# Optimization experiments

Hardware: AMD Instinct MI355X
Metric: run time of the kernel (lower is better)

## Reference

```python
import jax, jax.numpy as jnp
import numpy as np
from jax import lax

N = 100000      # nodes
F_IN = 128      # dataset.num_features
H = 64          # hidden
E = 1600000     # edges
G = 1000        # graphs (equal-sized, contiguous)
PER = N // G    # nodes per graph = 100
K = 30          # sort-pool k
KS = 3          # conv1d kernel = num_layers


def setup_inputs() -> dict:
    key = jax.random.key(0)
    ks = jax.random.split(key, 20)
    lin = lambda k, i, o: (jax.random.normal(k, (i, o), jnp.float32) / np.sqrt(i)).astype(jnp.float32)
    return {
        "x": jax.random.normal(ks[0], (N, F_IN), jnp.float32),
        "src": jax.random.randint(ks[1], (E,), 0, N, dtype=jnp.int32),
        "dst": jax.random.randint(ks[2], (E,), 0, N, dtype=jnp.int32),
        "num_graphs": G,
        # SAGEConv 1: lin_l (aggr, with bias), lin_r (self, no bias)
        "wl1": lin(ks[3], F_IN, H), "wr1": lin(ks[4], F_IN, H), "b1": jnp.zeros((H,), jnp.float32),
        "wl2": lin(ks[5], H, H), "wr2": lin(ks[6], H, H), "b2": jnp.zeros((H,), jnp.float32),
        "wl3": lin(ks[7], H, H), "wr3": lin(ks[8], H, H), "b3": jnp.zeros((H,), jnp.float32),
        # Conv1d(hidden=64 -> 32, kernel=3): weight [O, I, K]
        "cw": (jax.random.normal(ks[9], (32, H, KS), jnp.float32) / np.sqrt(H * KS)).astype(jnp.float32),
        "cb": jnp.zeros((32,), jnp.float32),
        "w1": lin(ks[10], 32 * (K - KS + 1), H), "bb1": jnp.zeros((H,), jnp.float32),
        "w2": lin(ks[11], H, 1), "bb2": jnp.zeros((1,), jnp.float32),
    }


def _sage(x, src, dst, wl, wr, b, n):
    # PyG SAGEConv (mean aggr): lin_l(mean_{j->i} x_j) + lin_r(x_i)
    msum = jax.ops.segment_sum(x[src], dst, num_segments=n)           # [N, F]
    cnt = jax.ops.segment_sum(jnp.ones((src.shape[0],), x.dtype), dst, num_segments=n)
    mean = msum / jnp.maximum(cnt, 1.0)[:, None]
    return mean @ wl + b + x @ wr


def reference(x, src, dst, num_graphs, wl1, wr1, b1, wl2, wr2, b2, wl3, wr3, b3, cw, cb, w1, bb1, w2, bb2):
    n = x.shape[0]
    h = jax.nn.relu(_sage(x, src, dst, wl1, wr1, b1, n))
    h = jax.nn.relu(_sage(h, src, dst, wl2, wr2, b2, n))
    h = jax.nn.relu(_sage(h, src, dst, wl3, wr3, b3, n))
    # SortAggregation(k): per-graph, sort nodes by last feature channel (desc), keep top-k.
    # batch = contiguous equal-sized graphs -> dense reshape is exact.
    hg = h.reshape(num_graphs, PER, H)                                # [G, PER, H]
    order = jnp.argsort(-hg[:, :, -1], axis=1)[:, :K]                 # [G, K]
    topk = jnp.take_along_axis(hg, order[:, :, None], axis=1)         # [G, K, H]
    xc = jnp.transpose(topk, (0, 2, 1))                               # [G, H, K]
    y = lax.conv_general_dilated(xc, cw, (1,), 'VALID',
                                 dimension_numbers=('NCH', 'OIH', 'NCH'))
    y = jax.nn.relu(y + cb[None, :, None])                            # [G, 32, K-KS+1]
    y = y.reshape(num_graphs, -1)
    y = jax.nn.relu(y @ w1 + bb1)
    # dropout: eval mode -> identity
    return y @ w2 + bb2                                               # [G, 1]
```

## Files before the change

kernel.cpp:

```cpp
#include <hip/hip_runtime.h>

#define NN 100000
#define EE 1600000
#define GG 1000
#define PERG 100
#define KK 30
#define HH 64

#define NB 782
#define CAP 4096
#define CHB 4096
#define BUCKET_BLOCKS ((EE + CHB - 1) / CHB)
#define PROJ_BLOCKS ((NN + 127) / 128)
#define LAYER_BLOCKS ((NN + 63) / 64)

__device__ __forceinline__ void bucket_body(int bid, float* smem,
                                            const int* __restrict__ src,
                                            const int* __restrict__ dst,
                                            int* __restrict__ gcur,
                                            int* __restrict__ pairs) {
  int* lhist = (int*)smem;
  int* lbase = lhist + NB;
  int* lcur = lbase + NB;
  const int t = threadIdx.x;
  const int c0 = bid * CHB;
  const int c1 = min(c0 + CHB, EE);
  for (int b = t; b < NB; b += 256) {
    lhist[b] = 0;
    lcur[b] = 0;
  }
  __syncthreads();
  for (int e = c0 + t; e < c1; e += 256) atomicAdd(&lhist[dst[e] >> 7], 1);
  __syncthreads();
  for (int b = t; b < NB; b += 256) {
    int c = lhist[b];
    lbase[b] = c ? atomicAdd(&gcur[b], c) : 0;
  }
  __syncthreads();
  for (int e = c0 + t; e < c1; e += 256) {
    int d = dst[e];
    int b = d >> 7;
    int p = atomicAdd(&lcur[b], 1);
    pairs[b * CAP + lbase[b] + p] = (src[e] << 7) | (d & 127);
  }
}

template <int K>
__device__ __forceinline__ void proj_body(int bid, float* smem,
                                          const float* __restrict__ X,
                                          const float* __restrict__ WL,
                                          const float* __restrict__ WR,
                                          float* __restrict__ P,
                                          float* __restrict__ R) {
  constexpr int BM = 128, BK = 32, XSP = 36, WSP = 144;
  float* xs = smem;
  float* ws = smem + BM * XSP;
  const int t = threadIdx.x;
  const int row0 = bid * BM;
  const int tc = t & 15, tr = t >> 4;
  const int wcol = tc * 8 + (tc >> 2) * 4;

  float acc[8][8];
#pragma unroll
  for (int i = 0; i < 8; ++i)
#pragma unroll
    for (int j = 0; j < 8; ++j) acc[i][j] = 0.f;

  for (int k0 = 0; k0 < K; k0 += BK) {
    __syncthreads();
    for (int idx = t; idx < BM * 8; idx += 256) {
      int r = idx >> 3, c = idx & 7;
      int row = row0 + r;
      float4 v = make_float4(0.f, 0.f, 0.f, 0.f);
      if (row < NN) v = *reinterpret_cast<const float4*>(&X[(size_t)row * K + k0 + c * 4]);
      *reinterpret_cast<float4*>(&xs[r * XSP + c * 4]) = v;
    }
    for (int idx = t; idx < BK * 16; idx += 256) {
      int kr = idx >> 4, c4 = idx & 15;
      int gcl = c4 >> 1;
      int off = gcl * 8 + (gcl >> 2) * 4 + (c4 & 1) * 4;
      *reinterpret_cast<float4*>(&ws[kr * WSP + off]) =
          *reinterpret_cast<const float4*>(&WL[(k0 + kr) * 64 + c4 * 4]);
      int g2 = gcl + 8;
      int off2 = g2 * 8 + (g2 >> 2) * 4 + (c4 & 1) * 4;
      *reinterpret_cast<float4*>(&ws[kr * WSP + off2]) =
          *reinterpret_cast<const float4*>(&WR[(k0 + kr) * 64 + c4 * 4]);
    }
    __syncthreads();
    for (int kk4 = 0; kk4 < BK; kk4 += 4) {
      float4 a[8];
#pragma unroll
      for (int i = 0; i < 8; ++i)
        a[i] = *reinterpret_cast<const float4*>(&xs[(tr + 16 * i) * XSP + kk4]);
#pragma unroll
      for (int kk = 0; kk < 4; ++kk) {
        float4 b0 = *reinterpret_cast<const float4*>(&ws[(kk4 + kk) * WSP + wcol]);
        float4 b1 = *reinterpret_cast<const float4*>(&ws[(kk4 + kk) * WSP + wcol + 4]);
        float bv[8] = {b0.x, b0.y, b0.z, b0.w, b1.x, b1.y, b1.z, b1.w};
#pragma unroll
        for (int i = 0; i < 8; ++i) {
          float av = (kk == 0) ? a[i].x : (kk == 1) ? a[i].y : (kk == 2) ? a[i].z : a[i].w;
#pragma unroll
          for (int j = 0; j < 8; ++j) acc[i][j] = fmaf(av, bv[j], acc[i][j]);
        }
      }
    }
  }

  float* OUT = (tc < 8) ? P : R;
  int cb = (tc & 7) * 8;
#pragma unroll
  for (int i = 0; i < 8; ++i) {
    int row = row0 + tr + 16 * i;
    if (row < NN) {
      *reinterpret_cast<float4*>(&OUT[(size_t)row * 64 + cb]) =
          make_float4(acc[i][0], acc[i][1], acc[i][2], acc[i][3]);
      *reinterpret_cast<float4*>(&OUT[(size_t)row * 64 + cb + 4]) =
          make_float4(acc[i][4], acc[i][5], acc[i][6], acc[i][7]);
    }
  }
}

__global__ __launch_bounds__(256) void fused_bucket_proj(const int* __restrict__ src,
                                                         const int* __restrict__ dst,
                                                         int* __restrict__ gcur,
                                                         int* __restrict__ pairs,
                                                         const float* __restrict__ X,
                                                         const float* __restrict__ WL,
                                                         const float* __restrict__ WR,
                                                         float* __restrict__ P,
                                                         float* __restrict__ R) {
  __shared__ float smem[128 * 36 + 32 * 144];
  if (blockIdx.x < PROJ_BLOCKS)
    proj_body<128>(blockIdx.x, smem, X, WL, WR, P, R);
  else
    bucket_body(blockIdx.x - PROJ_BLOCKS, smem, src, dst, gcur, pairs);
}

__global__ __launch_bounds__(256) void csr_kernel(const int* __restrict__ gcur,
                                                  const int* __restrict__ pairs,
                                                  int* __restrict__ row_start,
                                                  int* __restrict__ cnt,
                                                  int* __restrict__ eidx) {
  __shared__ int vals[CAP];
  __shared__ int hist[128];
  __shared__ int offs[128];
  __shared__ int cur[128];
  __shared__ int red[4];
  const int b = blockIdx.x;
  const int t = threadIdx.x;
  int s = 0;
  for (int i = t; i < b; i += 256) s += gcur[i];
#pragma unroll
  for (int off = 32; off > 0; off >>= 1) s += __shfl_xor(s, off);
  if ((t & 63) == 0) red[t >> 6] = s;
  if (t < 128) {
    hist[t] = 0;
    cur[t] = 0;
  }
  __syncthreads();
  const int base = red[0] + red[1] + red[2] + red[3];
  const int nb = gcur[b];
  for (int i = t; i < nb; i += 256) {
    int v = pairs[b * CAP + i];
    vals[i] = v;
    atomicAdd(&hist[v & 127], 1);
  }
  __syncthreads();
  if (t < 128) {
    int ss = 0;
    for (int m = 0; m < t; ++m) ss += hist[m];
    offs[t] = ss;
    int node = b * 128 + t;
    if (node < NN) {
      row_start[node] = base + ss;
      cnt[node] = hist[t];
    }
  }
  __syncthreads();
  for (int i = t; i < nb; i += 256) {
    int v = vals[i];
    int ld = v & 127;
    int p = atomicAdd(&cur[ld], 1);
    eidx[base + offs[ld] + p] = v >> 7;
  }
}

__global__ __launch_bounds__(256) void layer_kernel(const float* __restrict__ P,
                                                    const float* __restrict__ R,
                                                    const float* __restrict__ bias,
                                                    const int* __restrict__ row_start,
                                                    const int* __restrict__ cnt,
                                                    const int* __restrict__ eidx,
                                                    const float* __restrict__ WL,
                                                    const float* __restrict__ WR,
                                                    float* __restrict__ Pout,
                                                    float* __restrict__ Rout,
                                                    float* __restrict__ keyP,
                                                    float* __restrict__ keyR) {
  __shared__ float hs[64 * 68];
  const int t = threadIdx.x;
  const int lane = t & 63;
  const int qd = t >> 4;
  const int ql = t & 15;
  const int row0 = blockIdx.x * 64;

  for (int p = 0; p < 4; ++p) {
    const int r = qd + 16 * p;
    const int node = row0 + r;
    float4 acc = make_float4(0.f, 0.f, 0.f, 0.f);
    if (node < NN) {
      const int base = row_start[node];
      const int deg = cnt[node];
      for (int e0 = 0; e0 < deg; e0 += 16) {
        const int rem = deg - e0;
        const int ii = (ql < rem) ? ql : (rem - 1);
        int idx = eidx[base + e0 + ii];
#pragma unroll
        for (int j = 0; j < 16; ++j) {
          const int sj = __shfl(idx, (lane & 48) | j);
          const float wj = (j < rem) ? 1.f : 0.f;
          const float4 vj = *reinterpret_cast<const float4*>(&P[(size_t)sj * 64 + ql * 4]);
          acc.x = fmaf(wj, vj.x, acc.x);
          acc.y = fmaf(wj, vj.y, acc.y);
          acc.z = fmaf(wj, vj.z, acc.z);
          acc.w = fmaf(wj, vj.w, acc.w);
        }
      }
      const float dv = fmaxf((float)deg, 1.0f);
      const float4 r4 = *reinterpret_cast<const float4*>(&R[(size_t)node * 64 + ql * 4]);
      const float4 b4 = *reinterpret_cast<const float4*>(&bias[ql * 4]);
      acc.x = fmaxf(acc.x / dv + b4.x + r4.x, 0.f);
      acc.y = fmaxf(acc.y / dv + b4.y + r4.y, 0.f);
      acc.z = fmaxf(acc.z / dv + b4.z + r4.z, 0.f);
      acc.w = fmaxf(acc.w / dv + b4.w + r4.w, 0.f);
    }
    *reinterpret_cast<float4*>(&hs[r * 68 + ql * 4]) = acc;
  }
  __syncthreads();

  const int tc = t & 15, tr = t >> 4;
  const float* WB = (tc < 8) ? WL : WR;
  const int wcolg = (tc & 7) * 8;

  float acc[4][8];
#pragma unroll
  for (int i = 0; i < 4; ++i)
#pragma unroll
    for (int j = 0; j < 8; ++j) acc[i][j] = 0.f;

  for (int kk4 = 0; kk4 < 64; kk4 += 4) {
    float4 a[4];
#pragma unroll
    for (int i = 0; i < 4; ++i)
      a[i] = *reinterpret_cast<const float4*>(&hs[(tr + 16 * i) * 68 + kk4]);
#pragma unroll
    for (int kk = 0; kk < 4; ++kk) {
      float4 b0 = *reinterpret_cast<const float4*>(&WB[(kk4 + kk) * 64 + wcolg]);
      float4 b1 = *reinterpret_cast<const float4*>(&WB[(kk4 + kk) * 64 + wcolg + 4]);
      float bv[8] = {b0.x, b0.y, b0.z, b0.w, b1.x, b1.y, b1.z, b1.w};
#pragma unroll
      for (int i = 0; i < 4; ++i) {
        float av = (kk == 0) ? a[i].x : (kk == 1) ? a[i].y : (kk == 2) ? a[i].z : a[i].w;
#pragma unroll
        for (int j = 0; j < 8; ++j) acc[i][j] = fmaf(av, bv[j], acc[i][j]);
      }
    }
  }

  float* OUT = (tc < 8) ? Pout : Rout;
  const int cb = (tc & 7) * 8;
#pragma unroll
  for (int i = 0; i < 4; ++i) {
    int row = row0 + tr + 16 * i;
    if (row < NN) {
      *reinterpret_cast<float4*>(&OUT[(size_t)row * 64 + cb]) =
          make_float4(acc[i][0], acc[i][1], acc[i][2], acc[i][3]);
      *reinterpret_cast<float4*>(&OUT[(size_t)row * 64 + cb + 4]) =
          make_float4(acc[i][4], acc[i][5], acc[i][6], acc[i][7]);
      if (keyP != nullptr && tc == 7) keyP[row] = acc[i][7];
      if (keyR != nullptr && tc == 15) keyR[row] = acc[i][7];
    }
  }
}

__global__ __launch_bounds__(256) void keys_kernel(const float* __restrict__ keyP,
                                                   const float* __restrict__ keyR,
                                                   const float* __restrict__ b3,
                                                   const int* __restrict__ row_start,
                                                   const int* __restrict__ cnt,
                                                   const int* __restrict__ eidx,
                                                   float* __restrict__ keys) {
  const int node = blockIdx.x * 256 + threadIdx.x;
  if (node >= NN) return;
  const int base = row_start[node];
  const int deg = cnt[node];
  float s = 0.f;
  for (int e0 = 0; e0 < deg; e0 += 16) {
    const int rem = deg - e0;
    int id[16];
#pragma unroll
    for (int k = 0; k < 16; ++k) id[k] = eidx[base + e0 + ((k < rem) ? k : rem - 1)];
    float v[16];
#pragma unroll
    for (int k = 0; k < 16; ++k) v[k] = keyP[id[k]];
#pragma unroll
    for (int k = 0; k < 16; ++k) s += (k < rem) ? v[k] : 0.f;
  }
  const float dv = fmaxf((float)deg, 1.f);
  keys[node] = fmaxf(s / dv + b3[63] + keyR[node], 0.f);
}

__global__ __launch_bounds__(256) void sel_gather(const float* __restrict__ P,
                                                  const float* __restrict__ R,
                                                  const float* __restrict__ bias,
                                                  const float* __restrict__ keysArr,
                                                  const int* __restrict__ row_start,
                                                  const int* __restrict__ cnt,
                                                  const int* __restrict__ eidx,
                                                  float* __restrict__ feat) {
  __shared__ float key[PERG];
  __shared__ int sel[32];
  const int g = blockIdx.x;
  const int t = threadIdx.x;
  if (t < PERG) key[t] = keysArr[g * PERG + t];
  __syncthreads();
  if (t < PERG) {
    float kv = key[t];
    int r = 0;
    for (int m = 0; m < PERG; ++m) {
      float km = key[m];
      r += (int)((km > kv) || (km == kv && m < t));
    }
    if (r < KK) sel[r] = t;
  }
  __syncthreads();

  const int lane = t & 63;
  const int qd = t >> 4;
  const int ql = t & 15;
  for (int p = 0; p < 2; ++p) {
    const int r = qd + 16 * p;
    if (r < KK) {
      const int node = g * PERG + sel[r];
      const int base = row_start[node];
      const int deg = cnt[node];
      float4 acc = make_float4(0.f, 0.f, 0.f, 0.f);
      for (int e0 = 0; e0 < deg; e0 += 16) {
        const int rem = deg - e0;
        const int ii = (ql < rem) ? ql : (rem - 1);
        int idx = eidx[base + e0 + ii];
#pragma unroll
        for (int j = 0; j < 16; ++j) {
          const int sj = __shfl(idx, (lane & 48) | j);
          const float wj = (j < rem) ? 1.f : 0.f;
          const float4 vj = *reinterpret_cast<const float4*>(&P[(size_t)sj * 64 + ql * 4]);
          acc.x = fmaf(wj, vj.x, acc.x);
          acc.y = fmaf(wj, vj.y, acc.y);
          acc.z = fmaf(wj, vj.z, acc.z);
          acc.w = fmaf(wj, vj.w, acc.w);
        }
      }
      const float dv = fmaxf((float)deg, 1.0f);
      const float4 r4 = *reinterpret_cast<const float4*>(&R[(size_t)node * 64 + ql * 4]);
      const float4 b4 = *reinterpret_cast<const float4*>(&bias[ql * 4]);
      float4 o;
      o.x = fmaxf(acc.x / dv + b4.x + r4.x, 0.f);
      o.y = fmaxf(acc.y / dv + b4.y + r4.y, 0.f);
      o.z = fmaxf(acc.z / dv + b4.z + r4.z, 0.f);
      o.w = fmaxf(acc.w / dv + b4.w + r4.w, 0.f);
      *reinterpret_cast<float4*>(&feat[((size_t)g * KK + r) * 64 + ql * 4]) = o;
    }
  }
}

__global__ __launch_bounds__(256) void head_kernel(const float* __restrict__ gfeat,
                                                   const float* __restrict__ cw,
                                                   const float* __restrict__ cb,
                                                   const float* __restrict__ w1,
                                                   const float* __restrict__ bb1,
                                                   const float* __restrict__ w2,
                                                   const float* __restrict__ bb2,
                                                   float* __restrict__ out) {
  __shared__ float feat[34 * 65];
  __shared__ float cwT[192 * 33];
  __shared__ float z[896];
  __shared__ float psum[256];
  const int g = blockIdx.x;
  const int t = threadIdx.x;

  for (int idx = t; idx < 32 * 192; idx += 256) {
    int o = idx / 192, k = idx % 192;
    cwT[k * 33 + o] = cw[idx];
  }
  for (int idx = t; idx < KK * HH; idx += 256) {
    int r = idx >> 6, f = idx & 63;
    feat[r * 65 + f] = gfeat[((size_t)g * KK + r) * 64 + f];
  }
  __syncthreads();

  {
    const int o = t & 31;
    const int pg = t >> 5;
    float zacc[4] = {0.f, 0.f, 0.f, 0.f};
    int i = 0, tt = 0;
    for (int k = 0; k < 192; ++k) {
      float c = cwT[k * 33 + o];
#pragma unroll
      for (int j = 0; j < 4; ++j) {
        int p = pg + 8 * j;
        zacc[j] = fmaf(c, feat[(p + tt) * 65 + i], zacc[j]);
      }
      if (++tt == 3) {
        tt = 0;
        ++i;
      }
    }
    float cbo = cb[o];
#pragma unroll
    for (int j = 0; j < 4; ++j) {
      int p = pg + 8 * j;
      if (p < 28) z[o * 28 + p] = fmaxf(zacc[j] + cbo, 0.f);
    }
  }
  __syncthreads();

  {
    const int hh = t & 63;
    const int quarter = t >> 6;
    const int q0 = quarter * 224;
    float acc = 0.f;
    for (int q = 0; q < 224; ++q)
      acc = fmaf(z[q0 + q], w1[(size_t)(q0 + q) * 64 + hh], acc);
    psum[t] = acc;
  }
  __syncthreads();

  if (t < 64) {
    float o1 = fmaxf(bb1[t] + psum[t] + psum[t + 64] + psum[t + 128] + psum[t + 192], 0.f);
    float v = o1 * w2[t];
#pragma unroll
    for (int off = 32; off > 0; off >>= 1) v += __shfl_down(v, off);
    if (t == 0) out[g] = v + bb2[0];
  }
}

extern "C" void kernel_launch(void* const* d_in, const int* in_sizes, int n_in,
                              void* d_out, int out_size, void* d_ws, size_t ws_size,
                              hipStream_t stream) {
  const float* x = (const float*)d_in[0];
  const int* src = (const int*)d_in[1];
  const int* dst = (const int*)d_in[2];
  const float* wl1 = (const float*)d_in[4];
  const float* wr1 = (const float*)d_in[5];
  const float* b1 = (const float*)d_in[6];
  const float* wl2 = (const float*)d_in[7];
  const float* wr2 = (const float*)d_in[8];
  const float* b2 = (const float*)d_in[9];
  const float* wl3 = (const float*)d_in[10];
  const float* wr3 = (const float*)d_in[11];
  const float* b3 = (const float*)d_in[12];
  const float* cw = (const float*)d_in[13];
  const float* cb = (const float*)d_in[14];
  const float* w1 = (const float*)d_in[15];
  const float* bb1 = (const float*)d_in[16];
  const float* w2 = (const float*)d_in[17];
  const float* bb2 = (const float*)d_in[18];
  float* out = (float*)d_out;

  char* w = (char*)d_ws;
  auto carve = [&](size_t bytes) {
    char* p = w;
    w += (bytes + 255) & ~(size_t)255;
    return p;
  };
  int* row_start = (int*)carve((size_t)NN * 4);
  int* cnt = (int*)carve((size_t)NN * 4);
  int* eidx = (int*)carve((size_t)EE * 4);
  float* P = (float*)carve((size_t)NN * 64 * 4);
  float* R = (float*)carve((size_t)NN * 64 * 4);
  float* P2 = (float*)carve((size_t)NN * 64 * 4);
  float* R2 = (float*)carve((size_t)NN * 64 * 4);
  float* keys = (float*)carve((size_t)NN * 4);
  float* keyP = (float*)carve((size_t)NN * 4);
  float* keyR = (float*)carve((size_t)NN * 4);
  float* feat = (float*)carve((size_t)GG * KK * HH * 4);
  int* gcur = (int*)carve((size_t)NB * 4);
  int* pairs = (int*)P2;

  hipMemsetAsync(gcur, 0, (size_t)NB * 4, stream);
  fused_bucket_proj<<<BUCKET_BLOCKS + PROJ_BLOCKS, 256, 0, stream>>>(
      src, dst, gcur, pairs, x, wl1, wr1, P, R);
  csr_kernel<<<NB, 256, 0, stream>>>(gcur, pairs, row_start, cnt, eidx);

  layer_kernel<<<LAYER_BLOCKS, 256, 0, stream>>>(P, R, b1, row_start, cnt, eidx,
                                                 wl2, wr2, P2, R2, nullptr, nullptr);
  layer_kernel<<<LAYER_BLOCKS, 256, 0, stream>>>(P2, R2, b2, row_start, cnt, eidx,
                                                 wl3, wr3, P, R, keyP, keyR);
  keys_kernel<<<(NN + 255) / 256, 256, 0, stream>>>(keyP, keyR, b3, row_start, cnt,
                                                    eidx, keys);
  sel_gather<<<GG, 256, 0, stream>>>(P, R, b3, keys, row_start, cnt, eidx, feat);
  head_kernel<<<GG, 256, 0, stream>>>(feat, cw, cb, w1, bb1, w2, bb2, out);
}
```

Baseline: 452.8 us.

## Fuse key computation, top-k gather and head into one kernel; store layer-3 P in fp16

```diff
diff --git a/kernel.cpp b/kernel.cpp
--- a/kernel.cpp
+++ b/kernel.cpp
@@ -13,6 +13,9 @@
 #define BUCKET_BLOCKS ((EE + CHB - 1) / CHB)
 #define PROJ_BLOCKS ((NN + 127) / 128)
 #define LAYER_BLOCKS ((NN + 63) / 64)
+
+typedef _Float16 half4_t __attribute__((ext_vector_type(4)));
+typedef _Float16 half8_t __attribute__((ext_vector_type(8)));
 
 __device__ __forceinline__ void bucket_body(int bid, float* smem,
                                             const int* __restrict__ src,
@@ -186,6 +189,7 @@
   }
 }
 
+template <bool HOUT>
 __global__ __launch_bounds__(256) void layer_kernel(const float* __restrict__ P,
                                                     const float* __restrict__ R,
                                                     const float* __restrict__ bias,
@@ -195,6 +199,7 @@
                                                     const float* __restrict__ WL,
                                                     const float* __restrict__ WR,
                                                     float* __restrict__ Pout,
+                                                    _Float16* __restrict__ PoutH,
                                                     float* __restrict__ Rout,
                                                     float* __restrict__ keyP,
                                                     float* __restrict__ keyR) {
@@ -268,63 +273,79 @@
     }
   }
 
-  float* OUT = (tc < 8) ? Pout : Rout;
   const int cb = (tc & 7) * 8;
-#pragma unroll
-  for (int i = 0; i < 4; ++i) {
-    int row = row0 + tr + 16 * i;
-    if (row < NN) {
-      *reinterpret_cast<float4*>(&OUT[(size_t)row * 64 + cb]) =
-          make_float4(acc[i][0], acc[i][1], acc[i][2], acc[i][3]);
-      *reinterpret_cast<float4*>(&OUT[(size_t)row * 64 + cb + 4]) =
-          make_float4(acc[i][4], acc[i][5], acc[i][6], acc[i][7]);
-      if (keyP != nullptr && tc == 7) keyP[row] = acc[i][7];
-      if (keyR != nullptr && tc == 15) keyR[row] = acc[i][7];
-    }
-  }
-}
-
-__global__ __launch_bounds__(256) void keys_kernel(const float* __restrict__ keyP,
-                                                   const float* __restrict__ keyR,
-                                                   const float* __restrict__ b3,
-                                                   const int* __restrict__ row_start,
-                                                   const int* __restrict__ cnt,
-                                                   const int* __restrict__ eidx,
-                                                   float* __restrict__ keys) {
-  const int node = blockIdx.x * 256 + threadIdx.x;
-  if (node >= NN) return;
-  const int base = row_start[node];
-  const int deg = cnt[node];
-  float s = 0.f;
-  for (int e0 = 0; e0 < deg; e0 += 16) {
-    const int rem = deg - e0;
-    int id[16];
-#pragma unroll
-    for (int k = 0; k < 16; ++k) id[k] = eidx[base + e0 + ((k < rem) ? k : rem - 1)];
-    float v[16];
-#pragma unroll
-    for (int k = 0; k < 16; ++k) v[k] = keyP[id[k]];
-#pragma unroll
-    for (int k = 0; k < 16; ++k) s += (k < rem) ? v[k] : 0.f;
-  }
-  const float dv = fmaxf((float)deg, 1.f);
-  keys[node] = fmaxf(s / dv + b3[63] + keyR[node], 0.f);
-}
-
-__global__ __launch_bounds__(256) void sel_gather(const float* __restrict__ P,
-                                                  const float* __restrict__ R,
-                                                  const float* __restrict__ bias,
-                                                  const float* __restrict__ keysArr,
-                                                  const int* __restrict__ row_start,
-                                                  const int* __restrict__ cnt,
-                                                  const int* __restrict__ eidx,
-                                                  float* __restrict__ feat) {
+  if (tc < 8) {
+#pragma unroll
+    for (int i = 0; i < 4; ++i) {
+      int row = row0 + tr + 16 * i;
+      if (row < NN) {
+        if (HOUT) {
+          half8_t hv;
+#pragma unroll
+          for (int j = 0; j < 8; ++j) hv[j] = (_Float16)acc[i][j];
+          *reinterpret_cast<half8_t*>(&PoutH[(size_t)row * 64 + cb]) = hv;
+          if (keyP != nullptr && tc == 7) keyP[row] = acc[i][7];
+        } else {
+          *reinterpret_cast<float4*>(&Pout[(size_t)row * 64 + cb]) =
+              make_float4(acc[i][0], acc[i][1], acc[i][2], acc[i][3]);
+          *reinterpret_cast<float4*>(&Pout[(size_t)row * 64 + cb + 4]) =
+              make_float4(acc[i][4], acc[i][5], acc[i][6], acc[i][7]);
+        }
+      }
+    }
+  } else {
+#pragma unroll
+    for (int i = 0; i < 4; ++i) {
+      int row = row0 + tr + 16 * i;
+      if (row < NN) {
+        *reinterpret_cast<float4*>(&Rout[(size_t)row * 64 + cb]) =
+            make_float4(acc[i][0], acc[i][1], acc[i][2], acc[i][3]);
+        *reinterpret_cast<float4*>(&Rout[(size_t)row * 64 + cb + 4]) =
+            make_float4(acc[i][4], acc[i][5], acc[i][6], acc[i][7]);
+        if (HOUT && keyR != nullptr && tc == 15) keyR[row] = acc[i][7];
+      }
+    }
+  }
+}
+
+__global__ __launch_bounds__(256) void sel_head(const _Float16* __restrict__ Ph,
+                                                const float* __restrict__ R,
+                                                const float* __restrict__ b3,
+                                                const float* __restrict__ keyP,
+                                                const float* __restrict__ keyR,
+                                                const int* __restrict__ row_start,
+                                                const int* __restrict__ cnt,
+                                                const int* __restrict__ eidx,
+                                                const float* __restrict__ cw,
+                                                const float* __restrict__ cb,
+                                                const float* __restrict__ w1,
+                                                const float* __restrict__ bb1,
+                                                const float* __restrict__ w2,
+                                                const float* __restrict__ bb2,
+                                                float* __restrict__ out) {
   __shared__ float key[PERG];
   __shared__ int sel[32];
+  __shared__ float feat[34 * 65];
+  __shared__ float cwT[192 * 33];
+  __shared__ float z[896];
+  __shared__ float psum[256];
   const int g = blockIdx.x;
   const int t = threadIdx.x;
-  if (t < PERG) key[t] = keysArr[g * PERG + t];
-  __syncthreads();
+
+  for (int idx = t; idx < 32 * 192; idx += 256) {
+    int o = idx / 192, k = idx % 192;
+    cwT[k * 33 + o] = cw[idx];
+  }
+  if (t < PERG) {
+    const int node = g * PERG + t;
+    const int base = row_start[node];
+    const int deg = cnt[node];
+    float s = 0.f;
+    for (int e = 0; e < deg; ++e) s += keyP[eidx[base + e]];
+    key[t] = fmaxf(s / fmaxf((float)deg, 1.f) + b3[63] + keyR[node], 0.f);
+  }
+  __syncthreads();
+
   if (t < PERG) {
     float kv = key[t];
     int r = 0;
@@ -354,48 +375,22 @@
         for (int j = 0; j < 16; ++j) {
           const int sj = __shfl(idx, (lane & 48) | j);
           const float wj = (j < rem) ? 1.f : 0.f;
-          const float4 vj = *reinterpret_cast<const float4*>(&P[(size_t)sj * 64 + ql * 4]);
-          acc.x = fmaf(wj, vj.x, acc.x);
-          acc.y = fmaf(wj, vj.y, acc.y);
-          acc.z = fmaf(wj, vj.z, acc.z);
-          acc.w = fmaf(wj, vj.w, acc.w);
+          const half4_t hv =
+              *reinterpret_cast<const half4_t*>(&Ph[(size_t)sj * 64 + ql * 4]);
+          acc.x = fmaf(wj, (float)hv.x, acc.x);
+          acc.y = fmaf(wj, (float)hv.y, acc.y);
+          acc.z = fmaf(wj, (float)hv.z, acc.z);
+          acc.w = fmaf(wj, (float)hv.w, acc.w);
         }
       }
       const float dv = fmaxf((float)deg, 1.0f);
       const float4 r4 = *reinterpret_cast<const float4*>(&R[(size_t)node * 64 + ql * 4]);
-      const float4 b4 = *reinterpret_cast<const float4*>(&bias[ql * 4]);
-      float4 o;
-      o.x = fmaxf(acc.x / dv + b4.x + r4.x, 0.f);
-      o.y = fmaxf(acc.y / dv + b4.y + r4.y, 0.f);
-      o.z = fmaxf(acc.z / dv + b4.z + r4.z, 0.f);
-      o.w = fmaxf(acc.w / dv + b4.w + r4.w, 0.f);
-      *reinterpret_cast<float4*>(&feat[((size_t)g * KK + r) * 64 + ql * 4]) = o;
-    }
-  }
-}
-
-__global__ __launch_bounds__(256) void head_kernel(const float* __restrict__ gfeat,
-                                                   const float* __restrict__ cw,
-                                                   const float* __restrict__ cb,
-                                                   const float* __restrict__ w1,
-                                                   const float* __restrict__ bb1,
-                                                   const float* __restrict__ w2,
-                                                   const float* __restrict__ bb2,
-                                                   float* __restrict__ out) {
-  __shared__ float feat[34 * 65];
-  __shared__ float cwT[192 * 33];
-  __shared__ float z[896];
-  __shared__ float psum[256];
-  const int g = blockIdx.x;
-  const int t = threadIdx.x;
-
-  for (int idx = t; idx < 32 * 192; idx += 256) {
-    int o = idx / 192, k = idx % 192;
-    cwT[k * 33 + o] = cw[idx];
-  }
-  for (int idx = t; idx < KK * HH; idx += 256) {
-    int r = idx >> 6, f = idx & 63;
-    feat[r * 65 + f] = gfeat[((size_t)g * KK + r) * 64 + f];
+      const float4 b4 = *reinterpret_cast<const float4*>(&b3[ql * 4]);
+      feat[r * 65 + ql * 4 + 0] = fmaxf(acc.x / dv + b4.x + r4.x, 0.f);
+      feat[r * 65 + ql * 4 + 1] = fmaxf(acc.y / dv + b4.y + r4.y, 0.f);
+      feat[r * 65 + ql * 4 + 2] = fmaxf(acc.z / dv + b4.z + r4.z, 0.f);
+      feat[r * 65 + ql * 4 + 3] = fmaxf(acc.w / dv + b4.w + r4.w, 0.f);
+    }
   }
   __syncthreads();
 
@@ -477,28 +472,25 @@
   int* row_start = (int*)carve((size_t)NN * 4);
   int* cnt = (int*)carve((size_t)NN * 4);
   int* eidx = (int*)carve((size_t)EE * 4);
-  float* P = (float*)carve((size_t)NN * 64 * 4);
-  float* R = (float*)carve((size_t)NN * 64 * 4);
+  float* P1 = (float*)carve((size_t)NN * 64 * 4);
+  float* R1 = (float*)carve((size_t)NN * 64 * 4);
   float* P2 = (float*)carve((size_t)NN * 64 * 4);
   float* R2 = (float*)carve((size_t)NN * 64 * 4);
-  float* keys = (float*)carve((size_t)NN * 4);
+  _Float16* PhF = (_Float16*)carve((size_t)NN * 64 * 2);
   float* keyP = (float*)carve((size_t)NN * 4);
   float* keyR = (float*)carve((size_t)NN * 4);
-  float* feat = (float*)carve((size_t)GG * KK * HH * 4);
   int* gcur = (int*)carve((size_t)NB * 4);
   int* pairs = (int*)P2;
 
   hipMemsetAsync(gcur, 0, (size_t)NB * 4, stream);
   fused_bucket_proj<<<BUCKET_BLOCKS + PROJ_BLOCKS, 256, 0, stream>>>(
-      src, dst, gcur, pairs, x, wl1, wr1, P, R);
+      src, dst, gcur, pairs, x, wl1, wr1, P1, R1);
   csr_kernel<<<NB, 256, 0, stream>>>(gcur, pairs, row_start, cnt, eidx);
 
-  layer_kernel<<<LAYER_BLOCKS, 256, 0, stream>>>(P, R, b1, row_start, cnt, eidx,
-                                                 wl2, wr2, P2, R2, nullptr, nullptr);
-  layer_kernel<<<LAYER_BLOCKS, 256, 0, stream>>>(P2, R2, b2, row_start, cnt, eidx,
-                                                 wl3, wr3, P, R, keyP, keyR);
-  keys_kernel<<<(NN + 255) / 256, 256, 0, stream>>>(keyP, keyR, b3, row_start, cnt,
-                                                    eidx, keys);
-  sel_gather<<<GG, 256, 0, stream>>>(P, R, b3, keys, row_start, cnt, eidx, feat);
-  head_kernel<<<GG, 256, 0, stream>>>(feat, cw, cb, w1, bb1, w2, bb2, out);
-}
+  layer_kernel<false><<<LAYER_BLOCKS, 256, 0, stream>>>(
+      P1, R1, b1, row_start, cnt, eidx, wl2, wr2, P2, nullptr, R2, nullptr, nullptr);
+  layer_kernel<true><<<LAYER_BLOCKS, 256, 0, stream>>>(
+      P2, R2, b2, row_start, cnt, eidx, wl3, wr3, nullptr, PhF, R1, keyP, keyR);
+  sel_head<<<GG, 256, 0, stream>>>(PhF, R1, b3, keyP, keyR, row_start, cnt, eidx,
+                                   cw, cb, w1, bb1, w2, bb2, out);
+}
```

After: 436.9 us. -3.5%, faster.
